# Kernel optimization log

Measured on AMD Instinct MI355X. Metric: run time of the kernel, lower is better.

Reference implementation:

```python
import jax, jax.numpy as jnp
import numpy as np

N, IN_DIM, OUT_DIM = 8192, 512, 256

def setup_inputs() -> dict:
    key = jax.random.key(0)
    k1, k2, k3, k4, k5 = jax.random.split(key, 5)
    feat = jax.random.normal(k1, (N, IN_DIM), dtype=jnp.float32)
    counting_attn = jax.random.uniform(k2, (N, N), dtype=jnp.float32)
    Wq = jax.random.normal(k3, (IN_DIM, OUT_DIM), dtype=jnp.float32) * (IN_DIM ** -0.5)
    Wk = jax.random.normal(k4, (IN_DIM, OUT_DIM), dtype=jnp.float32) * (IN_DIM ** -0.5)
    Wv = jax.random.normal(k5, (IN_DIM, OUT_DIM), dtype=jnp.float32) * (IN_DIM ** -0.5)
    return {"feat": feat, "counting_attn": counting_attn, "Wq": Wq, "Wk": Wk, "Wv": Wv}

def reference(feat, counting_attn, Wq, Wk, Wv):
    # eval mode: feat_drop / attn_drop are identity
    Q = feat @ Wq  # [N, D]
    K = feat @ Wk
    V = feat @ Wv
    scale = 1.0 / jnp.sqrt(jnp.float32(Q.shape[1]))
    logits = (Q @ K.T) * scale  # [N, N]
    logits = logits - jnp.max(logits, axis=1, keepdims=True)
    a_nomi = jnp.exp(logits) * counting_attn
    a_deno = jnp.sum(a_nomi, axis=1, keepdims=True)
    a_nor = a_nomi / (a_deno + 1e-9)
    ret = a_nor @ V  # [N, D]
    return jax.nn.elu(ret)
```

## Files before the change

### kernel.cpp

```cpp
#include <hip/hip_runtime.h>

typedef unsigned short u16;
typedef unsigned int u32;
typedef __attribute__((ext_vector_type(8))) __bf16 bf16x8;
typedef __attribute__((ext_vector_type(16))) float f32x16;

#define NN 8192
#define IND 512
#define DD 256
#define LN_K 0.00195122595f

__device__ __forceinline__ void gl_lds16(const void* g, void* l) {
  __builtin_amdgcn_global_load_lds((const __attribute__((address_space(1))) void*)g,
                                   (__attribute__((address_space(3))) void*)l, 16, 0, 0);
}
__device__ __forceinline__ u16 bf16_rne(float x) {
  u32 u = __float_as_uint(x);
  u += 0x7FFF + ((u >> 16) & 1);
  return (u16)(u >> 16);
}

__global__ __launch_bounds__(256) void wt_transpose(const float* __restrict__ Wq,
                                                    const float* __restrict__ Wk,
                                                    const float* __restrict__ Wv,
                                                    u16* __restrict__ WT) {
  const int o = blockIdx.y;
  const int k0 = blockIdx.x * 8;
  const int n = threadIdx.x;
  const float* W = (o == 0) ? Wq : ((o == 1) ? Wk : Wv);
  u32 pk[4];
#pragma unroll
  for (int g = 0; g < 4; ++g) {
    const float a = W[(size_t)(k0 + 2 * g) * DD + n];
    const float b = W[(size_t)(k0 + 2 * g + 1) * DD + n];
    pk[g] = (u32)bf16_rne(a) | ((u32)bf16_rne(b) << 16);
  }
  *(uint4*)(WT + (size_t)o * (DD * IND) + (size_t)n * IND + k0) =
      make_uint4(pk[0], pk[1], pk[2], pk[3]);
}

__global__ __launch_bounds__(256) void cvt_feat(const float* __restrict__ f,
                                                u16* __restrict__ fb) {
  const int i = (blockIdx.x * 256 + threadIdx.x) * 4;
  float4 v = *(const float4*)(f + i);
  u32 lo = (u32)bf16_rne(v.x) | ((u32)bf16_rne(v.y) << 16);
  u32 hi = (u32)bf16_rne(v.z) | ((u32)bf16_rne(v.w) << 16);
  *(uint2*)(fb + i) = make_uint2(lo, hi);
}

__global__ __launch_bounds__(256, 4) void proj_qkv(const u16* __restrict__ featb,
                                                   const u16* __restrict__ WT,
                                                   u16* __restrict__ Qs,
                                                   u16* __restrict__ Ks,
                                                   u16* __restrict__ VTs) {
  __shared__ u16 tl[4][32 * 40];
  const int mb = blockIdx.x, o = blockIdx.y;
  const int wave = threadIdx.x >> 6, lane = threadIdx.x & 63;
  const int mm = lane & 31, h = lane >> 5;
  const int m0 = mb * 32;
  const u16* wt = WT + o * (DD * IND);

  f32x16 acc[2];
#pragma unroll
  for (int t = 0; t < 2; ++t)
#pragma unroll
    for (int r = 0; r < 16; ++r) acc[t][r] = 0.f;

  for (int kc = 0; kc < 32; ++kc) {
    bf16x8 af = *(const bf16x8*)(featb + (size_t)(m0 + mm) * IND + kc * 16 + 8 * h);
#pragma unroll
    for (int t = 0; t < 2; ++t) {
      const int nt = wave * 2 + t;
      bf16x8 bf = *(const bf16x8*)(wt + (size_t)(nt * 32 + mm) * IND + kc * 16 + 8 * h);
      acc[t] = __builtin_amdgcn_mfma_f32_32x32x16_bf16(af, bf, acc[t], 0, 0, 0);
    }
  }

  if (o < 2) {
    const float sc = (o == 0) ? 0.0625f : 1.f;
    u16* dst = (o == 0) ? Qs : Ks;
#pragma unroll
    for (int t = 0; t < 2; ++t) {
      const int nt = wave * 2 + t;
#pragma unroll
      for (int r = 0; r < 16; ++r) {
        const int mrow = (r & 3) + 8 * (r >> 2) + 4 * h;
        dst[(size_t)(m0 + mrow) * DD + nt * 32 + mm] = bf16_rne(acc[t][r] * sc);
      }
    }
  } else {
    const int n2 = lane >> 1, mh = lane & 1;
#pragma unroll
    for (int t = 0; t < 2; ++t) {
      const int nt = wave * 2 + t;
#pragma unroll
      for (int r = 0; r < 16; r += 2) {
        const int mrow = (r & 3) + 8 * (r >> 2) + 4 * h;
        u32 pk = (u32)bf16_rne(acc[t][r]) | ((u32)bf16_rne(acc[t][r + 1]) << 16);
        *(u32*)(&tl[wave][mm * 40 + mrow]) = pk;
      }
      bf16x8 t0 = *(const bf16x8*)(&tl[wave][n2 * 40 + mh * 16]);
      bf16x8 t1 = *(const bf16x8*)(&tl[wave][n2 * 40 + mh * 16 + 8]);
      u16* gp = VTs + (size_t)(nt * 32 + n2) * NN + m0 + mh * 16;
      *(bf16x8*)(gp) = t0;
      *(bf16x8*)(gp + 8) = t1;
    }
  }
}

__global__ __launch_bounds__(256, 2) void flash_attn(const u16* __restrict__ Qs,
                                                     const u16* __restrict__ Ks,
                                                     const u16* __restrict__ VTs,
                                                     const float* __restrict__ cnt,
                                                     float* __restrict__ ml,
                                                     float* __restrict__ Op,
                                                     int jiters, int spl) {
  __shared__ u16 kl[2][8192];
  __shared__ u16 vl[2][8192];
  const int bid = blockIdx.x;
  const int lg = __ffs(spl) - 1;
  const int sp = bid & (spl - 1);
  const int rb = bid >> lg;
  const int wave = threadIdx.x >> 6, lane = threadIdx.x & 63;
  const int mm = lane & 31, h = lane >> 5;
  const int m0 = rb * 128 + wave * 32;
  const int jbase = sp * jiters * 32;
  const int off = (rb * 7) & (jiters - 1);

  bf16x8 qf[16];
  {
    const u16* qrow = Qs + (size_t)(m0 + mm) * DD;
#pragma unroll
    for (int c = 0; c < 16; ++c) qf[c] = *(const bf16x8*)(qrow + c * 16 + 8 * h);
  }
  f32x16 acc[8];
#pragma unroll
  for (int nt = 0; nt < 8; ++nt)
#pragma unroll
    for (int r = 0; r < 16; ++r) acc[nt][r] = 0.f;
  float m_run = -1e30f, l_run = 0.f;

  {
    const int j00 = jbase + off * 32;
#pragma unroll
    for (int ii = 0; ii < 4; ++ii) {
      const int w = wave * 4 + ii;
      const int L = w * 64 + lane;
      gl_lds16(Ks + (size_t)(j00 + (L & 31)) * DD + (L >> 5) * 8, (char*)kl + w * 1024);
      gl_lds16(VTs + (size_t)(L & 255) * NN + j00 + (L >> 8) * 8, (char*)vl + w * 1024);
    }
  }

  for (int t = 0; t < jiters; ++t) {
    const int jb = (t + off) & (jiters - 1);
    const int buf = t & 1;
    const int j0 = jbase + jb * 32;

    float cf[16];
    {
      const float* crow = cnt + (size_t)(m0 + mm) * NN + j0 + 4 * h;
#pragma unroll
      for (int g = 0; g < 4; ++g) {
        float4 t4 = *(const float4*)(crow + 8 * g);
        cf[4 * g + 0] = t4.x;
        cf[4 * g + 1] = t4.y;
        cf[4 * g + 2] = t4.z;
        cf[4 * g + 3] = t4.w;
      }
    }

    asm volatile("s_waitcnt vmcnt(4)" ::: "memory");
    __builtin_amdgcn_s_barrier();
    asm volatile("" ::: "memory");

    if (t + 1 < jiters) {
      const int jn = jbase + ((t + 1 + off) & (jiters - 1)) * 32;
#pragma unroll
      for (int ii = 0; ii < 4; ++ii) {
        const int w = wave * 4 + ii;
        const int L = w * 64 + lane;
        gl_lds16(Ks + (size_t)(jn + (L & 31)) * DD + (L >> 5) * 8,
                 (char*)kl + (buf ^ 1) * 16384 + w * 1024);
        gl_lds16(VTs + (size_t)(L & 255) * NN + jn + (L >> 8) * 8,
                 (char*)vl + (buf ^ 1) * 16384 + w * 1024);
      }
    }

    const char* klb = (const char*)kl + buf * 16384;
    const char* vlb = (const char*)vl + buf * 16384;
    f32x16 sv0, sv1;
#pragma unroll
    for (int r = 0; r < 16; ++r) { sv0[r] = 0.f; sv1[r] = 0.f; }
    __builtin_amdgcn_s_setprio(1);
#pragma unroll
    for (int c = 0; c < 16; c += 2) {
      bf16x8 kf0 = *(const bf16x8*)(klb + (((2 * c + h) * 32 + mm) << 4));
      bf16x8 kf1 = *(const bf16x8*)(klb + (((2 * c + 2 + h) * 32 + mm) << 4));
      sv0 = __builtin_amdgcn_mfma_f32_32x32x16_bf16(kf0, qf[c], sv0, 0, 0, 0);
      sv1 = __builtin_amdgcn_mfma_f32_32x32x16_bf16(kf1, qf[c + 1], sv1, 0, 0, 0);
    }
    __builtin_amdgcn_s_setprio(0);
    f32x16 sv = sv0 + sv1;

    float ma = fmaxf(fmaxf(sv[0], sv[1]), sv[2]);
    float mb2 = fmaxf(fmaxf(sv[3], sv[4]), sv[5]);
    float mc = fmaxf(fmaxf(sv[6], sv[7]), sv[8]);
    float md = fmaxf(fmaxf(sv[9], sv[10]), sv[11]);
    float me = fmaxf(fmaxf(sv[12], sv[13]), sv[14]);
    float mx = fmaxf(fmaxf(fmaxf(ma, mb2), mc), fmaxf(fmaxf(md, me), sv[15]));
    mx = fmaxf(mx, __shfl_xor(mx, 32));

    const bool upd = __any(mx > m_run + 8.f);
    if (upd) {
      const float m_new = fmaxf(m_run, mx);
      const float alpha = __expf(m_run - m_new);
      l_run *= alpha;
#pragma unroll
      for (int nt = 0; nt < 8; ++nt)
#pragma unroll
        for (int r = 0; r < 16; ++r) acc[nt][r] *= alpha;
      m_run = m_new;
    }
    const float msub = m_run - LN_K;

    float p[16];
#pragma unroll
    for (int r = 0; r < 16; ++r) p[r] = __expf(sv[r] - msub) * cf[r];
    float s0 = (p[0] + p[1]) + (p[2] + p[3]);
    float s1 = (p[4] + p[5]) + (p[6] + p[7]);
    float s2 = (p[8] + p[9]) + (p[10] + p[11]);
    float s3 = (p[12] + p[13]) + (p[14] + p[15]);
    float bsum = (s0 + s1) + (s2 + s3);
    bsum += __shfl_xor(bsum, 32);
    l_run += bsum;

    u32 P2[8];
#pragma unroll
    for (int j = 0; j < 8; ++j) {
      const u32 ua = __float_as_uint(p[2 * j]);
      const u32 ub = __float_as_uint(p[2 * j + 1]);
      P2[j] = (ua >> 16) | (ub & 0xFFFF0000u);
    }
#pragma unroll
    for (int kc2 = 0; kc2 < 2; ++kc2) {
      union { u32 u[4]; bf16x8 v; } pf;
#pragma unroll
      for (int tp = 0; tp < 4; ++tp) {
        const int src = mm + 32 * (tp >> 1);
        const u32 va = __shfl(P2[4 * kc2 + (tp & 1)], src);
        const u32 vb = __shfl(P2[4 * kc2 + 2 + (tp & 1)], src);
        pf.u[tp] = h ? vb : va;
      }
      __builtin_amdgcn_s_setprio(1);
#pragma unroll
      for (int nt = 0; nt < 8; ++nt) {
        bf16x8 vf = *(const bf16x8*)(vlb + ((((2 * kc2 + h) * 256) + nt * 32 + mm) << 4));
        acc[nt] = __builtin_amdgcn_mfma_f32_32x32x16_bf16(vf, pf.v, acc[nt], 0, 0, 0);
      }
      __builtin_amdgcn_s_setprio(0);
    }
  }

  const int wb = rb * 4 + wave;
  if (lane < 32) {
    ml[((sp * 256 + wb) << 6) + lane] = m_run;
    ml[((sp * 256 + wb) << 6) + 32 + lane] = l_run;
  }
#pragma unroll
  for (int nt = 0; nt < 8; ++nt) {
#pragma unroll
    for (int rr = 0; rr < 4; ++rr) {
      float* op = Op + ((((size_t)(sp * 256 + wb) * 8 + nt) * 4 + rr) * 64 + lane) * 4;
      float4 v = make_float4(acc[nt][4 * rr], acc[nt][4 * rr + 1],
                             acc[nt][4 * rr + 2], acc[nt][4 * rr + 3]);
      *(float4*)op = v;
    }
  }
}

template <int SPL>
__global__ __launch_bounds__(256) void merge_out(const float* __restrict__ ml,
                                                 const float* __restrict__ Op,
                                                 float* __restrict__ out) {
  const int wid = blockIdx.x * 4 + (threadIdx.x >> 6);
  const int lane = threadIdx.x & 63, mm = lane & 31, h = lane >> 5;
  const int wb = wid >> 3, nt = wid & 7;
  float mv[SPL], lv[SPL], wsc[SPL];
#pragma unroll
  for (int s = 0; s < SPL; ++s) {
    mv[s] = ml[((s * 256 + wb) << 6) + mm];
    lv[s] = ml[((s * 256 + wb) << 6) + 32 + mm];
  }
  float M = mv[0];
#pragma unroll
  for (int s = 1; s < SPL; ++s) M = fmaxf(M, mv[s]);
  float L = 0.f;
#pragma unroll
  for (int s = 0; s < SPL; ++s) {
    wsc[s] = __expf(mv[s] - M);
    L += wsc[s] * lv[s];
  }
  const float inv = 1.f / (L + 1e-9f);

  float o[16];
#pragma unroll
  for (int r = 0; r < 16; ++r) o[r] = 0.f;
#pragma unroll
  for (int s = 0; s < SPL; ++s) {
#pragma unroll
    for (int rr = 0; rr < 4; ++rr) {
      const float* op = Op + ((((size_t)(s * 256 + wb) * 8 + nt) * 4 + rr) * 64 + lane) * 4;
      float4 v = *(const float4*)op;
      o[4 * rr + 0] += wsc[s] * v.x;
      o[4 * rr + 1] += wsc[s] * v.y;
      o[4 * rr + 2] += wsc[s] * v.z;
      o[4 * rr + 3] += wsc[s] * v.w;
    }
  }
  const int row = wb * 32 + mm;
#pragma unroll
  for (int g = 0; g < 4; ++g) {
    float4 v;
    float* pv = &v.x;
#pragma unroll
    for (int i = 0; i < 4; ++i) {
      float t = o[4 * g + i] * inv;
      pv[i] = t > 0.f ? t : expm1f(t);
    }
    *(float4*)(out + (size_t)row * DD + nt * 32 + 8 * g + 4 * h) = v;
  }
}

extern "C" void kernel_launch(void* const* d_in, const int* in_sizes, int n_in,
                              void* d_out, int out_size, void* d_ws, size_t ws_size,
                              hipStream_t stream) {
  const float* feat = (const float*)d_in[0];
  const float* cnta = (const float*)d_in[1];
  const float* Wq = (const float*)d_in[2];
  const float* Wk = (const float*)d_in[3];
  const float* Wv = (const float*)d_in[4];
  char* ws = (char*)d_ws;
  u16* WT = (u16*)(ws);
  u16* featb = (u16*)(ws + (1ull << 20));
  u16* Qs = (u16*)(ws + (9ull << 20));
  u16* Ks = (u16*)(ws + (13ull << 20));
  u16* VTs = (u16*)(ws + (17ull << 20));
  float* ml = (float*)(ws + (21ull << 20));
  float* Op = (float*)(ws + (22ull << 20));
  float* out = (float*)d_out;

  const size_t need8 = (22ull << 20) + (64ull << 20);
  const int spl = (ws_size >= need8) ? 8 : 4;
  const int jiters = NN / (spl * 32);

  hipLaunchKernelGGL(wt_transpose, dim3(64, 3), dim3(256), 0, stream, Wq, Wk, Wv, WT);
  hipLaunchKernelGGL(cvt_feat, dim3(4096), dim3(256), 0, stream, feat, featb);
  hipLaunchKernelGGL(proj_qkv, dim3(256, 3), dim3(256), 0, stream, featb, WT, Qs, Ks, VTs);
  hipLaunchKernelGGL(flash_attn, dim3(64 * spl), dim3(256), 0, stream, Qs, Ks, VTs, cnta, ml,
                     Op, jiters, spl);
  if (spl == 8) {
    hipLaunchKernelGGL((merge_out<8>), dim3(512), dim3(256), 0, stream, ml, Op, out);
  } else {
    hipLaunchKernelGGL((merge_out<4>), dim3(512), dim3(256), 0, stream, ml, Op, out);
  }
}
```

Baseline: 538.5 us.

## Double the flash_attn block to 8 waves and prefetch counting_attn via LDS

Blocks grow from 4 to 8 waves (256 query rows each), so every K/V tile staged in LDS is shared by twice as many rows and each wave issues half as many K/V async loads. The counting_attn tile is now prefetched one iteration ahead with global_load_lds into a double-buffered LDS region, instead of being loaded into registers right before use. This aims to hide counting_attn load latency and cut K/V global traffic. In exchange it uses 128KB of dynamic LDS per block, halves the grid, and relies on fragile hand-written vmcnt wait counts.

```diff
diff --git a/kernel.cpp b/kernel.cpp
--- a/kernel.cpp
+++ b/kernel.cpp
@@ -108,24 +108,27 @@
   }
 }
 
-__global__ __launch_bounds__(256, 2) void flash_attn(const u16* __restrict__ Qs,
+__global__ __launch_bounds__(512, 2) void flash_attn(const u16* __restrict__ Qs,
                                                      const u16* __restrict__ Ks,
                                                      const u16* __restrict__ VTs,
                                                      const float* __restrict__ cnt,
                                                      float* __restrict__ ml,
                                                      float* __restrict__ Op,
                                                      int jiters, int spl) {
-  __shared__ u16 kl[2][8192];
-  __shared__ u16 vl[2][8192];
+  extern __shared__ char smem[];
+  char* kl = smem;
+  char* vl = smem + 32768;
+  char* cfl = smem + 65536;
   const int bid = blockIdx.x;
   const int lg = __ffs(spl) - 1;
   const int sp = bid & (spl - 1);
   const int rb = bid >> lg;
   const int wave = threadIdx.x >> 6, lane = threadIdx.x & 63;
   const int mm = lane & 31, h = lane >> 5;
-  const int m0 = rb * 128 + wave * 32;
+  const int m0 = rb * 256 + wave * 32;
   const int jbase = sp * jiters * 32;
   const int off = (rb * 7) & (jiters - 1);
+  const float* crow = cnt + (size_t)(m0 + mm) * NN + 4 * h;
 
   bf16x8 qf[16];
   {
@@ -143,31 +146,22 @@
   {
     const int j00 = jbase + off * 32;
 #pragma unroll
-    for (int ii = 0; ii < 4; ++ii) {
-      const int w = wave * 4 + ii;
+    for (int ii = 0; ii < 2; ++ii) {
+      const int w = wave * 2 + ii;
       const int L = w * 64 + lane;
-      gl_lds16(Ks + (size_t)(j00 + (L & 31)) * DD + (L >> 5) * 8, (char*)kl + w * 1024);
-      gl_lds16(VTs + (size_t)(L & 255) * NN + j00 + (L >> 8) * 8, (char*)vl + w * 1024);
-    }
+      gl_lds16(Ks + (size_t)(j00 + (L & 31)) * DD + (L >> 5) * 8, kl + w * 1024);
+      gl_lds16(VTs + (size_t)(L & 255) * NN + j00 + (L >> 8) * 8, vl + w * 1024);
+    }
+#pragma unroll
+    for (int ii = 0; ii < 4; ++ii)
+      gl_lds16(crow + j00 + 8 * ii, cfl + wave * 4096 + ii * 1024);
   }
 
   for (int t = 0; t < jiters; ++t) {
     const int jb = (t + off) & (jiters - 1);
     const int buf = t & 1;
     const int j0 = jbase + jb * 32;
-
-    float cf[16];
-    {
-      const float* crow = cnt + (size_t)(m0 + mm) * NN + j0 + 4 * h;
-#pragma unroll
-      for (int g = 0; g < 4; ++g) {
-        float4 t4 = *(const float4*)(crow + 8 * g);
-        cf[4 * g + 0] = t4.x;
-        cf[4 * g + 1] = t4.y;
-        cf[4 * g + 2] = t4.z;
-        cf[4 * g + 3] = t4.w;
-      }
-    }
+    (void)j0;
 
     asm volatile("s_waitcnt vmcnt(4)" ::: "memory");
     __builtin_amdgcn_s_barrier();
@@ -176,18 +170,21 @@
     if (t + 1 < jiters) {
       const int jn = jbase + ((t + 1 + off) & (jiters - 1)) * 32;
 #pragma unroll
-      for (int ii = 0; ii < 4; ++ii) {
-        const int w = wave * 4 + ii;
+      for (int ii = 0; ii < 2; ++ii) {
+        const int w = wave * 2 + ii;
         const int L = w * 64 + lane;
         gl_lds16(Ks + (size_t)(jn + (L & 31)) * DD + (L >> 5) * 8,
-                 (char*)kl + (buf ^ 1) * 16384 + w * 1024);
+                 kl + (buf ^ 1) * 16384 + w * 1024);
         gl_lds16(VTs + (size_t)(L & 255) * NN + jn + (L >> 8) * 8,
-                 (char*)vl + (buf ^ 1) * 16384 + w * 1024);
-      }
-    }
-
-    const char* klb = (const char*)kl + buf * 16384;
-    const char* vlb = (const char*)vl + buf * 16384;
+                 vl + (buf ^ 1) * 16384 + w * 1024);
+      }
+#pragma unroll
+      for (int ii = 0; ii < 4; ++ii)
+        gl_lds16(crow + jn + 8 * ii, cfl + (buf ^ 1) * 32768 + wave * 4096 + ii * 1024);
+    }
+
+    const char* klb = kl + buf * 16384;
+    const char* vlb = vl + buf * 16384;
     f32x16 sv0, sv1;
 #pragma unroll
     for (int r = 0; r < 16; ++r) { sv0[r] = 0.f; sv1[r] = 0.f; }
@@ -201,6 +198,23 @@
     }
     __builtin_amdgcn_s_setprio(0);
     f32x16 sv = sv0 + sv1;
+
+    if (t + 1 < jiters)
+      asm volatile("s_waitcnt vmcnt(8)" ::: "memory");
+    else
+      asm volatile("s_waitcnt vmcnt(0)" ::: "memory");
+    float cf[16];
+    {
+      const char* cfb = cfl + buf * 32768 + wave * 4096 + h * 512 + mm * 16;
+#pragma unroll
+      for (int g = 0; g < 4; ++g) {
+        float4 t4 = *(const float4*)(cfb + g * 1024);
+        cf[4 * g + 0] = t4.x;
+        cf[4 * g + 1] = t4.y;
+        cf[4 * g + 2] = t4.z;
+        cf[4 * g + 3] = t4.w;
+      }
+    }
 
     float ma = fmaxf(fmaxf(sv[0], sv[1]), sv[2]);
     float mb2 = fmaxf(fmaxf(sv[3], sv[4]), sv[5]);
@@ -261,7 +275,7 @@
     }
   }
 
-  const int wb = rb * 4 + wave;
+  const int wb = rb * 8 + wave;
   if (lane < 32) {
     ml[((sp * 256 + wb) << 6) + lane] = m_run;
     ml[((sp * 256 + wb) << 6) + 32 + lane] = l_run;
@@ -353,11 +367,18 @@
   const int spl = (ws_size >= need8) ? 8 : 4;
   const int jiters = NN / (spl * 32);
 
+  static bool attr_set = false;
+  if (!attr_set) {
+    (void)hipFuncSetAttribute((const void*)flash_attn,
+                              hipFuncAttributeMaxDynamicSharedMemorySize, 131072);
+    attr_set = true;
+  }
+
   hipLaunchKernelGGL(wt_transpose, dim3(64, 3), dim3(256), 0, stream, Wq, Wk, Wv, WT);
   hipLaunchKernelGGL(cvt_feat, dim3(4096), dim3(256), 0, stream, feat, featb);
   hipLaunchKernelGGL(proj_qkv, dim3(256, 3), dim3(256), 0, stream, featb, WT, Qs, Ks, VTs);
-  hipLaunchKernelGGL(flash_attn, dim3(64 * spl), dim3(256), 0, stream, Qs, Ks, VTs, cnta, ml,
-                     Op, jiters, spl);
+  hipLaunchKernelGGL(flash_attn, dim3(32 * spl), dim3(512), 131072, stream, Qs, Ks, VTs,
+                     cnta, ml, Op, jiters, spl);
   if (spl == 8) {
     hipLaunchKernelGGL((merge_out<8>), dim3(512), dim3(256), 0, stream, ml, Op, out);
   } else {
```

Result: faster. 475.7 us (-11.7%).
